# Optimization experiments

Hardware: AMD Instinct MI355X
Metric: run time of the kernel (lower is better)

The kernel has to match this reference:

```python
import jax, jax.numpy as jnp
import numpy as np


def setup_inputs() -> dict:
    key = jax.random.key(0)
    k1, k2, k3 = jax.random.split(key, 3)
    B, E, L, D = 32, 256, 2048, 256
    doc_state = jax.random.normal(k1, (B, L, D), dtype=jnp.float32)
    entity_mapping = jax.random.uniform(k2, (B, E, L), dtype=jnp.float32)
    entity_lens = jax.random.uniform(k3, (B, E), dtype=jnp.float32)
    return {"doc_state": doc_state, "entity_mapping": entity_mapping, "entity_lens": entity_lens}


def reference(doc_state, entity_mapping, entity_lens):
    # Original: (entity_mapping[:, :, :, None] * doc_state[:, None, :, :]).sum(2) / entity_lens[:, :, None]
    # This is a batched contraction over L; express as einsum to avoid the
    # huge [B, E, L, D] intermediate.
    summed = jnp.einsum('bel,bld->bed', entity_mapping, doc_state)  # [B, E, D]
    return summed / entity_lens[:, :, None]
```

## Files before the change

### kernel.cpp

```cpp
#include <hip/hip_runtime.h>
#include <stdint.h>

#define B_ 32
#define E_ 256
#define L_ 2048
#define D_ 256

#define BE 128
#define BD 256
#define BK 32
#define KS 4
#define KCHUNK (L_ / KS)
#define NKT (KCHUNK / BK)

typedef __attribute__((ext_vector_type(2))) float  f32x2;
typedef __attribute__((ext_vector_type(4))) float  f32x4;
typedef __attribute__((ext_vector_type(4))) short  s16x4;
typedef __attribute__((ext_vector_type(8))) short  s16x8;

#define KEYA(row) ((((row) >> 1) & 3) | (((row) & 1) << 2))
#define KEYB(row) (((row) >> 1) & 7)

__device__ __forceinline__ void cvt_hilo1(float x, short &h, short &l) {
    unsigned u = __builtin_bit_cast(unsigned, x);
    h = (short)(u >> 16);
    float hf = __builtin_bit_cast(float, u & 0xFFFF0000u);
    unsigned r = __builtin_bit_cast(unsigned, x - hf);
    l = (short)(r >> 16);
}

__global__ void zero_out_kernel(f32x4* __restrict__ out) {
    out[(size_t)blockIdx.x * 256 + threadIdx.x] = f32x4{0.f, 0.f, 0.f, 0.f};
}

__global__ __launch_bounds__(512, 2)
void mean_pool_kernel(const float* __restrict__ doc,
                      const float* __restrict__ emap,
                      const float* __restrict__ lens,
                      float* __restrict__ out) {
    __shared__ __align__(16) short As[2][BE][64];
    __shared__ __align__(16) short Bs[2][BD][64];
    __shared__ float lens_s[BE];

    const int t   = threadIdx.x;
    const int blk = blockIdx.x;
    const int ks  = blk & 3;
    const int e0  = ((blk >> 2) & 1) * BE;
    const int b   = blk >> 3;

    const float* Ag = emap + ((size_t)b * E_ + e0) * L_ + ks * KCHUNK;
    const float* Sg = doc  + (size_t)b * L_ * D_ + (size_t)ks * KCHUNK * D_;

    if (t < BE) lens_s[t] = lens[b * E_ + e0 + t];

    const int a_c4 = t & 7;
    const int a_r  = t >> 3;
    const int dp   = t & 127;
    const int kb   = t >> 7;

    const int lane = t & 63;
    const int w    = t >> 6;
    const int eo   = (w & 1) * 64;
    const int dq   = (w >> 1) * 64;
    const int ml   = lane & 15;
    const int kg   = lane >> 4;

    int awo_h[2], awo_l[2];
    #pragma unroll
    for (int rr = 0; rr < 2; ++rr) {
        const int row = a_r + rr * 64, k = KEYA(row), hb = (a_c4 & 1) * 4;
        awo_h[rr] = row * 64 + ((((a_c4 >> 1)    ) ^ k) << 3) + hb;
        awo_l[rr] = row * 64 + ((((a_c4 >> 1) | 4) ^ k) << 3) + hb;
    }
    int bwo_h[2], bwo_l[2];
    #pragma unroll
    for (int dd = 0; dd < 2; ++dd) {
        const int row = dp * 2 + dd, k = KEYB(row);
        bwo_h[dd] = row * 64 + (((kb    ) ^ k) << 3);
        bwo_l[dd] = row * 64 + (((kb | 4) ^ k) << 3);
    }
    int aro_h[4], aro_l[4], bro_h[4], bro_l[4];
    #pragma unroll
    for (int i = 0; i < 4; ++i) {
        const int ar = eo + i * 16 + ml, ka = KEYA(ar);
        aro_h[i] = ar * 64 + (((kg    ) ^ ka) << 3);
        aro_l[i] = ar * 64 + (((kg | 4) ^ ka) << 3);
        const int br = dq + i * 16 + ml, kB = KEYB(br);
        bro_h[i] = br * 64 + (((kg    ) ^ kB) << 3);
        bro_l[i] = br * 64 + (((kg | 4) ^ kB) << 3);
    }

    f32x4 acc[4][4] = {};
    f32x4 pa[2];
    f32x2 pb[8];

    #pragma unroll
    for (int rr = 0; rr < 2; ++rr)
        pa[rr] = *(const f32x4*)(Ag + (size_t)(a_r + rr * 64) * L_ + a_c4 * 4);
    #pragma unroll
    for (int j = 0; j < 8; ++j)
        pb[j] = *(const f32x2*)(Sg + (size_t)(kb * 8 + j) * D_ + dp * 2);

    #pragma unroll 2
    for (int kt = 0; kt < NKT; ++kt) {
        short* Ab = &As[kt & 1][0][0];
        short* Bb = &Bs[kt & 1][0][0];

        #pragma unroll
        for (int rr = 0; rr < 2; ++rr) {
            s16x4 h, l;
            #pragma unroll
            for (int i = 0; i < 4; ++i) { short hh, ll; cvt_hilo1(pa[rr][i], hh, ll); h[i] = hh; l[i] = ll; }
            *(s16x4*)&Ab[awo_h[rr]] = h;
            *(s16x4*)&Ab[awo_l[rr]] = l;
        }
        #pragma unroll
        for (int dd = 0; dd < 2; ++dd) {
            s16x8 h, l;
            #pragma unroll
            for (int j = 0; j < 8; ++j) { short hh, ll; cvt_hilo1(pb[j][dd], hh, ll); h[j] = hh; l[j] = ll; }
            *(s16x8*)&Bb[bwo_h[dd]] = h;
            *(s16x8*)&Bb[bwo_l[dd]] = l;
        }
        __syncthreads();

        if (kt + 1 < NKT) {
            const int k0 = (kt + 1) * BK;
            #pragma unroll
            for (int rr = 0; rr < 2; ++rr)
                pa[rr] = *(const f32x4*)(Ag + (size_t)(a_r + rr * 64) * L_ + k0 + a_c4 * 4);
            #pragma unroll
            for (int j = 0; j < 8; ++j)
                pb[j] = *(const f32x2*)(Sg + (size_t)(k0 + kb * 8 + j) * D_ + dp * 2);
        }

        s16x8 bh[4], bl[4];
        #pragma unroll
        for (int ni = 0; ni < 4; ++ni) {
            bh[ni] = *(const s16x8*)&Bb[bro_h[ni]];
            bl[ni] = *(const s16x8*)&Bb[bro_l[ni]];
        }
        __builtin_amdgcn_s_setprio(1);
        #pragma unroll
        for (int mi = 0; mi < 4; ++mi) {
            const s16x8 ah = *(const s16x8*)&Ab[aro_h[mi]];
            const s16x8 al = *(const s16x8*)&Ab[aro_l[mi]];
            #pragma unroll
            for (int ni = 0; ni < 4; ++ni) {
                acc[mi][ni] = __builtin_amdgcn_mfma_f32_16x16x32_bf16(ah, bh[ni], acc[mi][ni], 0, 0, 0);
                acc[mi][ni] = __builtin_amdgcn_mfma_f32_16x16x32_bf16(ah, bl[ni], acc[mi][ni], 0, 0, 0);
                acc[mi][ni] = __builtin_amdgcn_mfma_f32_16x16x32_bf16(al, bh[ni], acc[mi][ni], 0, 0, 0);
            }
        }
        __builtin_amdgcn_s_setprio(0);
    }

    #pragma unroll
    for (int mi = 0; mi < 4; ++mi) {
        #pragma unroll
        for (int rr = 0; rr < 4; ++rr) {
            const int er = eo + mi * 16 + kg * 4 + rr;
            const float lv = lens_s[er];
            #pragma unroll
            for (int ni = 0; ni < 4; ++ni)
                atomicAdd(&out[((size_t)(b * E_ + e0 + er)) * D_ + dq + ni * 16 + ml],
                          acc[mi][ni][rr] / lv);
        }
    }
}

extern "C" void kernel_launch(void* const* d_in, const int* in_sizes, int n_in,
                              void* d_out, int out_size, void* d_ws, size_t ws_size,
                              hipStream_t stream) {
    const float* doc  = (const float*)d_in[0];
    const float* emap = (const float*)d_in[1];
    const float* lens = (const float*)d_in[2];
    float* out = (float*)d_out;

    zero_out_kernel<<<dim3(out_size / (4 * 256)), dim3(256), 0, stream>>>((f32x4*)out);

    dim3 grid(B_ * (E_ / BE) * (D_ / BD) * KS);
    dim3 block(512);
    hipLaunchKernelGGL(mean_pool_kernel, grid, block, 0, stream,
                       doc, emap, lens, out);
}
```

Baseline: 177.9 us.

## Deepen register prefetch to two tiles and use single barrier per K-step

Restructures the main loop into a manually unrolled ping-pong pipeline. Global loads now run two tiles ahead in two register sets, and the next tile's bf16 hi/lo conversion and LDS store overlap with the current tile's MFMAs. All LDS fragments are read into registers before the stage writes, and each step ends with one lgkmcnt-wait plus barrier instead of a __syncthreads before compute. This aims to hide global latency and conversion cost behind MFMA work, at the cost of more registers with 2 waves/SIMD launch bounds.

```diff
diff --git a/kernel.cpp b/kernel.cpp
--- a/kernel.cpp
+++ b/kernel.cpp
@@ -32,6 +32,73 @@
 __global__ void zero_out_kernel(f32x4* __restrict__ out) {
     out[(size_t)blockIdx.x * 256 + threadIdx.x] = f32x4{0.f, 0.f, 0.f, 0.f};
 }
+
+#define LOADT(PA, PB, K0)                                                      \
+    {                                                                          \
+        _Pragma("unroll")                                                      \
+        for (int rr = 0; rr < 2; ++rr)                                         \
+            PA[rr] = *(const f32x4*)(Ag + (size_t)(a_r + rr * 64) * L_ + (K0) + a_c4 * 4); \
+        _Pragma("unroll")                                                      \
+        for (int j = 0; j < 8; ++j)                                            \
+            PB[j] = *(const f32x2*)(Sg + (size_t)((K0) + kb * 8 + j) * D_ + dp * 2); \
+    }
+
+#define STAGE_CONV(AbN, BbN, PA, PB)                                           \
+    {                                                                          \
+        _Pragma("unroll")                                                      \
+        for (int rr = 0; rr < 2; ++rr) {                                       \
+            s16x4 h, l;                                                        \
+            _Pragma("unroll")                                                  \
+            for (int i = 0; i < 4; ++i) { short hh, ll; cvt_hilo1(PA[rr][i], hh, ll); h[i] = hh; l[i] = ll; } \
+            *(s16x4*)&(AbN)[awo_h[rr]] = h;                                    \
+            *(s16x4*)&(AbN)[awo_l[rr]] = l;                                    \
+        }                                                                      \
+        _Pragma("unroll")                                                      \
+        for (int dd = 0; dd < 2; ++dd) {                                       \
+            s16x8 h, l;                                                        \
+            _Pragma("unroll")                                                  \
+            for (int j = 0; j < 8; ++j) { short hh, ll; cvt_hilo1(PB[j][dd], hh, ll); h[j] = hh; l[j] = ll; } \
+            *(s16x8*)&(BbN)[bwo_h[dd]] = h;                                    \
+            *(s16x8*)&(BbN)[bwo_l[dd]] = l;                                    \
+        }                                                                      \
+    }
+
+#define LGKM_BARRIER()                                                         \
+    {                                                                          \
+        asm volatile("s_waitcnt lgkmcnt(0)" ::: "memory");                     \
+        __builtin_amdgcn_s_barrier();                                          \
+        asm volatile("" ::: "memory");                                         \
+    }
+
+#define ITER(K, AbC, BbC, AbN, BbN, PA, PB)                                    \
+    {                                                                          \
+        s16x8 bh[4], bl[4], ah[4], al[4];                                      \
+        _Pragma("unroll")                                                      \
+        for (int ni = 0; ni < 4; ++ni) {                                       \
+            bh[ni] = *(const s16x8*)&(BbC)[bro_h[ni]];                         \
+            bl[ni] = *(const s16x8*)&(BbC)[bro_l[ni]];                         \
+        }                                                                      \
+        _Pragma("unroll")                                                      \
+        for (int mi = 0; mi < 4; ++mi) {                                       \
+            ah[mi] = *(const s16x8*)&(AbC)[aro_h[mi]];                         \
+            al[mi] = *(const s16x8*)&(AbC)[aro_l[mi]];                         \
+        }                                                                      \
+        if ((K) + 1 < NKT) {                                                   \
+            STAGE_CONV(AbN, BbN, PA, PB)                                       \
+            if ((K) + 3 < NKT) LOADT(PA, PB, ((K) + 3) * BK)                   \
+        }                                                                      \
+        __builtin_amdgcn_s_setprio(1);                                         \
+        _Pragma("unroll")                                                      \
+        for (int mi = 0; mi < 4; ++mi)                                         \
+            _Pragma("unroll")                                                  \
+            for (int ni = 0; ni < 4; ++ni) {                                   \
+                acc[mi][ni] = __builtin_amdgcn_mfma_f32_16x16x32_bf16(ah[mi], bh[ni], acc[mi][ni], 0, 0, 0); \
+                acc[mi][ni] = __builtin_amdgcn_mfma_f32_16x16x32_bf16(ah[mi], bl[ni], acc[mi][ni], 0, 0, 0); \
+                acc[mi][ni] = __builtin_amdgcn_mfma_f32_16x16x32_bf16(al[mi], bh[ni], acc[mi][ni], 0, 0, 0); \
+            }                                                                  \
+        __builtin_amdgcn_s_setprio(0);                                         \
+        if ((K) + 1 < NKT) LGKM_BARRIER()                                      \
+    }
 
 __global__ __launch_bounds__(512, 2)
 void mean_pool_kernel(const float* __restrict__ doc,
@@ -91,68 +158,18 @@
     }
 
     f32x4 acc[4][4] = {};
-    f32x4 pa[2];
-    f32x2 pb[8];
-
-    #pragma unroll
-    for (int rr = 0; rr < 2; ++rr)
-        pa[rr] = *(const f32x4*)(Ag + (size_t)(a_r + rr * 64) * L_ + a_c4 * 4);
-    #pragma unroll
-    for (int j = 0; j < 8; ++j)
-        pb[j] = *(const f32x2*)(Sg + (size_t)(kb * 8 + j) * D_ + dp * 2);
-
-    #pragma unroll 2
-    for (int kt = 0; kt < NKT; ++kt) {
-        short* Ab = &As[kt & 1][0][0];
-        short* Bb = &Bs[kt & 1][0][0];
-
-        #pragma unroll
-        for (int rr = 0; rr < 2; ++rr) {
-            s16x4 h, l;
-            #pragma unroll
-            for (int i = 0; i < 4; ++i) { short hh, ll; cvt_hilo1(pa[rr][i], hh, ll); h[i] = hh; l[i] = ll; }
-            *(s16x4*)&Ab[awo_h[rr]] = h;
-            *(s16x4*)&Ab[awo_l[rr]] = l;
-        }
-        #pragma unroll
-        for (int dd = 0; dd < 2; ++dd) {
-            s16x8 h, l;
-            #pragma unroll
-            for (int j = 0; j < 8; ++j) { short hh, ll; cvt_hilo1(pb[j][dd], hh, ll); h[j] = hh; l[j] = ll; }
-            *(s16x8*)&Bb[bwo_h[dd]] = h;
-            *(s16x8*)&Bb[bwo_l[dd]] = l;
-        }
-        __syncthreads();
-
-        if (kt + 1 < NKT) {
-            const int k0 = (kt + 1) * BK;
-            #pragma unroll
-            for (int rr = 0; rr < 2; ++rr)
-                pa[rr] = *(const f32x4*)(Ag + (size_t)(a_r + rr * 64) * L_ + k0 + a_c4 * 4);
-            #pragma unroll
-            for (int j = 0; j < 8; ++j)
-                pb[j] = *(const f32x2*)(Sg + (size_t)(k0 + kb * 8 + j) * D_ + dp * 2);
-        }
-
-        s16x8 bh[4], bl[4];
-        #pragma unroll
-        for (int ni = 0; ni < 4; ++ni) {
-            bh[ni] = *(const s16x8*)&Bb[bro_h[ni]];
-            bl[ni] = *(const s16x8*)&Bb[bro_l[ni]];
-        }
-        __builtin_amdgcn_s_setprio(1);
-        #pragma unroll
-        for (int mi = 0; mi < 4; ++mi) {
-            const s16x8 ah = *(const s16x8*)&Ab[aro_h[mi]];
-            const s16x8 al = *(const s16x8*)&Ab[aro_l[mi]];
-            #pragma unroll
-            for (int ni = 0; ni < 4; ++ni) {
-                acc[mi][ni] = __builtin_amdgcn_mfma_f32_16x16x32_bf16(ah, bh[ni], acc[mi][ni], 0, 0, 0);
-                acc[mi][ni] = __builtin_amdgcn_mfma_f32_16x16x32_bf16(ah, bl[ni], acc[mi][ni], 0, 0, 0);
-                acc[mi][ni] = __builtin_amdgcn_mfma_f32_16x16x32_bf16(al, bh[ni], acc[mi][ni], 0, 0, 0);
-            }
-        }
-        __builtin_amdgcn_s_setprio(0);
+    f32x4 paE[2], paO[2];
+    f32x2 pbE[8], pbO[8];
+
+    LOADT(paE, pbE, 0)
+    LOADT(paO, pbO, BK)
+    STAGE_CONV(&As[0][0][0], &Bs[0][0][0], paE, pbE)
+    LOADT(paE, pbE, 2 * BK)
+    LGKM_BARRIER()
+
+    for (int kt = 0; kt < NKT; kt += 2) {
+        ITER(kt,     (&As[0][0][0]), (&Bs[0][0][0]), (&As[1][0][0]), (&Bs[1][0][0]), paO, pbO)
+        ITER(kt + 1, (&As[1][0][0]), (&Bs[1][0][0]), (&As[0][0][0]), (&Bs[0][0][0]), paE, pbE)
     }
 
     #pragma unroll
```

Result: no change. 176.8 us (-0.6%).
